# Performance work log

Hardware: AMD Instinct MI355X
Metric: run time of the kernel (lower is better)

## Reference

```python
import jax, jax.numpy as jnp
import numpy as np

B, T, V, E, H, L = 2, 1024, 32000, 768, 12, 4
HD = E // H
STD = 0.02


def setup_inputs() -> dict:
    key = jax.random.key(0)
    ks = jax.random.split(key, 16)
    inp = {}
    for i in range(L + 1):
        inp[f"t{i}"] = jax.random.randint(ks[i], (B, T), 0, V)
    inp["wte"] = jax.random.normal(ks[5], (V, E)) * STD
    inp["wpe"] = jax.random.normal(ks[6], (T, E)) * STD
    inp["ln1_w"] = jnp.ones((L, E)); inp["ln1_b"] = jnp.zeros((L, E))
    inp["ln2_w"] = jnp.ones((L, E)); inp["ln2_b"] = jnp.zeros((L, E))
    inp["attn_w"] = jax.random.normal(ks[7], (L, E, 3 * E)) * STD
    inp["attn_b"] = jnp.zeros((L, 3 * E))
    # c_proj has NANOGPT_SCALE_INIT -> std scaled by (2*L)**-0.5
    inp["proj_w"] = jax.random.normal(ks[8], (L, E, E)) * (STD * (2 * L) ** (-0.5))
    inp["proj_b"] = jnp.zeros((L, E))
    inp["fc1_w"] = jax.random.normal(ks[9], (L, E, 3 * E)) * STD
    inp["fc1_b"] = jnp.zeros((L, 3 * E))
    inp["fc2_w"] = jax.random.normal(ks[10], (L, 3 * E, E)) * STD
    inp["fc2_b"] = jnp.zeros((L, E))
    return inp


def _layernorm(x, w, b):
    mu = x.mean(-1, keepdims=True)
    var = ((x - mu) ** 2).mean(-1, keepdims=True)
    return (x - mu) / jnp.sqrt(var + 1e-5) * w + b


def _block(x, i, ln1_w, ln1_b, ln2_w, ln2_b, attn_w, attn_b, proj_w, proj_b, fc1_w, fc1_b, fc2_w, fc2_b):
    h = _layernorm(x, ln1_w[i], ln1_b[i])
    qkv = h @ attn_w[i] + attn_b[i]                       # [B,T,3E]
    q, k, v = jnp.split(qkv, 3, axis=-1)
    q = q.reshape(B, T, H, HD); k = k.reshape(B, T, H, HD); v = v.reshape(B, T, H, HD)
    # FAITHFUL quirk: original divides by d**(-0.5) == multiply by sqrt(d); no causal mask applied
    att = jnp.einsum('bqhd,bkhd->bhqk', q, k) * (HD ** 0.5)
    att = jax.nn.softmax(att, axis=-1)
    y = jnp.einsum('bhqk,bkhd->bqhd', att, v).reshape(B, T, E)
    x = x + y @ proj_w[i] + proj_b[i]
    h2 = _layernorm(x, ln2_w[i], ln2_b[i])
    return x + jax.nn.gelu(h2 @ fc1_w[i] + fc1_b[i], approximate=True) @ fc2_w[i] + fc2_b[i]


def reference(t0, t1, t2, t3, t4, wte, wpe, ln1_w, ln1_b, ln2_w, ln2_b,
              attn_w, attn_b, proj_w, proj_b, fc1_w, fc1_b, fc2_w, fc2_b):
    targets = [t0, t1, t2, t3, t4]
    pos = wpe[:T]                                         # [T,E]
    loss = jnp.float32(0.0)
    logits = None
    for i in range(L):
        x = wte[targets[i]] + pos                         # fresh embedding each layer (per original)
        x = _block(x, i, ln1_w, ln1_b, ln2_w, ln2_b, attn_w, attn_b,
                   proj_w, proj_b, fc1_w, fc1_b, fc2_w, fc2_b)
        logits = x @ wte.T                                # tied lm_head, no bias
        logp = jax.nn.log_softmax(logits, axis=-1)
        loss = loss + (-jnp.take_along_axis(logp, targets[i + 1][..., None], axis=-1).mean())
    return logits, loss
```

## Files before the change

### kernel.cpp

```cpp
#include <hip/hip_runtime.h>
#include <hip/hip_bf16.h>
#include <math.h>

#define BB 2
#define TT 1024
#define VV 32000
#define EE 768
#define HH 12
#define LL 4
#define HDIM 64
#define BT (BB*TT)
#define E3 (3*EE)

typedef __hip_bfloat16 bf16;
typedef __attribute__((ext_vector_type(8))) short bf16x8;
typedef __attribute__((ext_vector_type(4))) float f32x4;

__device__ __forceinline__ float bf2f(bf16 v) { return __bfloat162float(v); }
__device__ __forceinline__ bf16 f2bf(float v) { return __float2bfloat16(v); }

__device__ __forceinline__ void async_load16(const void* g, void* l) {
  __builtin_amdgcn_global_load_lds((const __attribute__((address_space(1))) void*)g,
                                   (__attribute__((address_space(3))) void*)l, 16, 0, 0);
}

__device__ __forceinline__ float gelu_tanh(float x) {
  float u = 0.7978845608028654f * (x + 0.044715f * x * x * x);
  return 0.5f * x * (1.0f + tanhf(u));
}


__global__ void detect_kernel(const unsigned* __restrict__ raw, int* flag, int force_bf16) {
  if (force_bf16) { *flag = 0; return; }
  *flag = (raw[0] == 0x3F800000u && raw[1] == 0x3F800000u) ? 1 : 0;
}

__global__ __launch_bounds__(256) void convert_kernel(const void* __restrict__ in,
                                                      bf16* __restrict__ out, long n,
                                                      const int* __restrict__ flag) {
  long i = (long)blockIdx.x * 256 + threadIdx.x;
  if (i >= n) return;
  int f = *flag;
  out[i] = f ? f2bf(((const float*)in)[i]) : ((const bf16*)in)[i];
}

__global__ void zero_loss_kernel(float* p) { *p = 0.f; }

__global__ void write_loss_kernel(const float* p, void* out, const int* flag) {
  if (*flag) ((float*)out)[(size_t)BT * VV] = *p;
  else       ((bf16*)out)[(size_t)BT * VV] = f2bf(*p);
}

__global__ __launch_bounds__(256) void transpose_kernel(const void* __restrict__ in,
                                                        bf16* __restrict__ out,
                                                        int R, int C, int layer,
                                                        const int* __restrict__ flag) {
  __shared__ bf16 tile[32][33];
  int f = *flag;
  const float* inf = (const float*)in + (size_t)layer * R * C;
  const bf16* inb  = (const bf16*)in  + (size_t)layer * R * C;
  int r0 = blockIdx.y * 32, c0 = blockIdx.x * 32;
#pragma unroll
  for (int i = 0; i < 4; ++i) {
    size_t idx = (size_t)(r0 + threadIdx.y + i * 8) * C + c0 + threadIdx.x;
    tile[threadIdx.y + i * 8][threadIdx.x] = f ? f2bf(inf[idx]) : inb[idx];
  }
  __syncthreads();
#pragma unroll
  for (int i = 0; i < 4; ++i) {
    int c = c0 + threadIdx.y + i * 8;
    out[(size_t)c * R + r0 + threadIdx.x] = tile[threadIdx.x][threadIdx.y + i * 8];
  }
}


__global__ __launch_bounds__(256) void embed_kernel(const int* __restrict__ tok,
                                                    const bf16* __restrict__ wte,
                                                    const bf16* __restrict__ wpe,
                                                    float* __restrict__ x) {
  int r = blockIdx.x;
  int tk = tok[r];
  int t = r & (TT - 1);
#pragma unroll
  for (int i = 0; i < 3; ++i) {
    int e = threadIdx.x + i * 256;
    x[(size_t)r * EE + e] = bf2f(wte[(size_t)tk * EE + e]) + bf2f(wpe[(size_t)t * EE + e]);
  }
}

__global__ __launch_bounds__(256) void ln_kernel(const float* __restrict__ x,
                                                 const bf16* __restrict__ wgt,
                                                 const bf16* __restrict__ bia,
                                                 bf16* __restrict__ out) {
  int r = blockIdx.x;
  const float* xr = x + (size_t)r * EE;
  int tid = threadIdx.x;
  float v0 = xr[tid], v1 = xr[tid + 256], v2 = xr[tid + 512];
  float s = v0 + v1 + v2;
  for (int o = 1; o < 64; o <<= 1) s += __shfl_xor(s, o, 64);
  __shared__ float red[4];
  int wv = tid >> 6;
  if ((tid & 63) == 0) red[wv] = s;
  __syncthreads();
  float mu = (red[0] + red[1] + red[2] + red[3]) * (1.f / 768.f);
  __syncthreads();
  float d0 = v0 - mu, d1 = v1 - mu, d2 = v2 - mu;
  float q = d0 * d0 + d1 * d1 + d2 * d2;
  for (int o = 1; o < 64; o <<= 1) q += __shfl_xor(q, o, 64);
  if ((tid & 63) == 0) red[wv] = q;
  __syncthreads();
  float var = (red[0] + red[1] + red[2] + red[3]) * (1.f / 768.f);
  float rs = rsqrtf(var + 1e-5f);
  bf16* orow = out + (size_t)r * EE;
  orow[tid]       = f2bf(d0 * rs * bf2f(wgt[tid])       + bf2f(bia[tid]));
  orow[tid + 256] = f2bf(d1 * rs * bf2f(wgt[tid + 256]) + bf2f(bia[tid + 256]));
  orow[tid + 512] = f2bf(d2 * rs * bf2f(wgt[tid + 512]) + bf2f(bia[tid + 512]));
}

__global__ __launch_bounds__(256) void split_qkv_kernel(const bf16* __restrict__ qkv,
                                                        bf16* __restrict__ Q,
                                                        bf16* __restrict__ Km,
                                                        bf16* __restrict__ Vt) {
  int idx = blockIdx.x * 256 + threadIdx.x;
  int r = idx / E3, c = idx % E3;
  int sec = c / EE, e = c % EE;
  int h = e >> 6, d = e & 63;
  int b = r >> 10, t = r & 1023;
  int bh = b * HH + h;
  bf16 v = qkv[(size_t)idx];
  if (sec == 0)      Q[((size_t)bh * TT + t) * HDIM + d] = v;
  else if (sec == 1) Km[((size_t)bh * TT + t) * HDIM + d] = v;
  else               Vt[((size_t)bh * HDIM + d) * TT + t] = v;
}


template<int BM, int BN>
__global__ __launch_bounds__(256) void gemm_bt(const bf16* __restrict__ A,
                                               const bf16* __restrict__ Bt,
                                               const bf16* __restrict__ bias,
                                               bf16* __restrict__ outb,
                                               float* __restrict__ outf,
                                               const float* __restrict__ resid,
                                               int M, int N, int K, int gelu,
                                               const int* __restrict__ oflag) {
  constexpr int IT = BM / 32;
  constexpr int JT = BN / 32;
  constexpr int ACH = BM / 64;
  constexpr int BCH = BN / 64;
  __shared__ __attribute__((aligned(16))) bf16 As[BM * 32];
  __shared__ __attribute__((aligned(16))) bf16 Bs[BN * 32];
  int f32o = (oflag != nullptr) && (*oflag != 0);
  int tid = threadIdx.x;
  int wave = tid >> 6, lane = tid & 63, low = lane & 15, quad = lane >> 4;
  int m0 = blockIdx.y * BM, n0 = blockIdx.x * BN;
  int wm = (wave >> 1) * (BM / 2), wn = (wave & 1) * (BN / 2);
  f32x4 acc[IT][JT];
  f32x4 zero = {0.f, 0.f, 0.f, 0.f};
#pragma unroll
  for (int i = 0; i < IT; ++i)
#pragma unroll
    for (int j = 0; j < JT; ++j) acc[i][j] = zero;

  for (int kb = 0; kb < K; kb += 32) {
    __syncthreads();
#pragma unroll
    for (int c = 0; c < ACH; ++c) {
      int g = c * 256 + tid;
      async_load16(A + (size_t)(m0 + (g >> 2)) * K + kb + (g & 3) * 8, (char*)As + g * 16);
    }
#pragma unroll
    for (int c = 0; c < BCH; ++c) {
      int g = c * 256 + tid;
      async_load16(Bt + (size_t)(n0 + (g >> 2)) * K + kb + (g & 3) * 8, (char*)Bs + g * 16);
    }
    __syncthreads();
    bf16x8 af[IT], bfr[JT];
#pragma unroll
    for (int i = 0; i < IT; ++i)
      af[i] = *(const bf16x8*)(As + (wm + i * 16 + low) * 32 + quad * 8);
#pragma unroll
    for (int j = 0; j < JT; ++j)
      bfr[j] = *(const bf16x8*)(Bs + (wn + j * 16 + low) * 32 + quad * 8);
#pragma unroll
    for (int i = 0; i < IT; ++i)
#pragma unroll
      for (int j = 0; j < JT; ++j)
        acc[i][j] = __builtin_amdgcn_mfma_f32_16x16x32_bf16(af[i], bfr[j], acc[i][j], 0, 0, 0);
  }

#pragma unroll
  for (int i = 0; i < IT; ++i)
#pragma unroll
    for (int j = 0; j < JT; ++j)
#pragma unroll
      for (int r = 0; r < 4; ++r) {
        int m = m0 + wm + i * 16 + quad * 4 + r;
        int n = n0 + wn + j * 16 + low;
        float v = acc[i][j][r];
        if (bias) v += bf2f(bias[n]);
        if (gelu) v = gelu_tanh(v);
        size_t idx = (size_t)m * N + n;
        if (resid) v += resid[idx];
        if (outf) outf[idx] = v;
        if (outb) {
          if (f32o) ((float*)outb)[idx] = v;
          else      outb[idx] = f2bf(v);
        }
      }
}


__global__ __launch_bounds__(64) void attn_kernel(const bf16* __restrict__ Q,
                                                  const bf16* __restrict__ Km,
                                                  const bf16* __restrict__ Vt,
                                                  bf16* __restrict__ y) {
  __shared__ __attribute__((aligned(16))) bf16 plds[16 * 32];
  int bh = blockIdx.x >> 6;
  int q0 = (blockIdx.x & 63) << 4;
  int b = bh / HH, h = bh % HH;
  int lane = threadIdx.x, low = lane & 15, quad = lane >> 4;
  const bf16* Qb = Q + (size_t)bh * TT * HDIM;
  const bf16* Kb = Km + (size_t)bh * TT * HDIM;
  const bf16* Vb = Vt + (size_t)bh * HDIM * TT;

  bf16x8 aq0 = *(const bf16x8*)(Qb + (size_t)(q0 + low) * HDIM + quad * 8);
  bf16x8 aq1 = *(const bf16x8*)(Qb + (size_t)(q0 + low) * HDIM + 32 + quad * 8);

  f32x4 o[4];
  f32x4 zero = {0.f, 0.f, 0.f, 0.f};
  float mr[4], lr[4];
#pragma unroll
  for (int r = 0; r < 4; ++r) { o[r] = zero; mr[r] = -1e30f; lr[r] = 0.f; }

  for (int kt = 0; kt < TT; kt += 32) {
    bf16x8 bk00 = *(const bf16x8*)(Kb + (size_t)(kt + low) * HDIM + quad * 8);
    bf16x8 bk01 = *(const bf16x8*)(Kb + (size_t)(kt + low) * HDIM + 32 + quad * 8);
    bf16x8 bk10 = *(const bf16x8*)(Kb + (size_t)(kt + 16 + low) * HDIM + quad * 8);
    bf16x8 bk11 = *(const bf16x8*)(Kb + (size_t)(kt + 16 + low) * HDIM + 32 + quad * 8);
    f32x4 sa = zero, sb = zero;
    sa = __builtin_amdgcn_mfma_f32_16x16x32_bf16(aq0, bk00, sa, 0, 0, 0);
    sa = __builtin_amdgcn_mfma_f32_16x16x32_bf16(aq1, bk01, sa, 0, 0, 0);
    sb = __builtin_amdgcn_mfma_f32_16x16x32_bf16(aq0, bk10, sb, 0, 0, 0);
    sb = __builtin_amdgcn_mfma_f32_16x16x32_bf16(aq1, bk11, sb, 0, 0, 0);
#pragma unroll
    for (int r = 0; r < 4; ++r) {
      float s0 = sa[r] * 8.f, s1 = sb[r] * 8.f;
      float tm = fmaxf(s0, s1);
      for (int oo = 1; oo < 16; oo <<= 1) tm = fmaxf(tm, __shfl_xor(tm, oo, 64));
      float mn = fmaxf(mr[r], tm);
      float alpha = __expf(mr[r] - mn);
      float p0 = __expf(s0 - mn), p1 = __expf(s1 - mn);
      float rs = p0 + p1;
      for (int oo = 1; oo < 16; oo <<= 1) rs += __shfl_xor(rs, oo, 64);
      lr[r] = lr[r] * alpha + rs;
      mr[r] = mn;
      o[0][r] *= alpha; o[1][r] *= alpha; o[2][r] *= alpha; o[3][r] *= alpha;
      plds[(quad * 4 + r) * 32 + low] = f2bf(p0);
      plds[(quad * 4 + r) * 32 + 16 + low] = f2bf(p1);
    }
    __syncthreads();
    bf16x8 pa = *(const bf16x8*)(plds + low * 32 + quad * 8);
#pragma unroll
    for (int fb = 0; fb < 4; ++fb) {
      bf16x8 bv = *(const bf16x8*)(Vb + (size_t)(fb * 16 + low) * TT + kt + quad * 8);
      o[fb] = __builtin_amdgcn_mfma_f32_16x16x32_bf16(pa, bv, o[fb], 0, 0, 0);
    }
    __syncthreads();
  }
#pragma unroll
  for (int fb = 0; fb < 4; ++fb)
#pragma unroll
    for (int r = 0; r < 4; ++r) {
      float val = o[fb][r] / lr[r];
      y[(size_t)(b * TT + q0 + quad * 4 + r) * EE + h * HDIM + fb * 16 + low] = f2bf(val);
    }
}


__global__ __launch_bounds__(256) void loss_kernel(const void* __restrict__ logits,
                                                   const int* __restrict__ tgt,
                                                   float* __restrict__ acc,
                                                   const int* __restrict__ flag) {
  int r = blockIdx.x;
  int f = *flag;
  const bf16* rowb = (const bf16*)logits + (size_t)r * VV;
  const float* rowf = (const float*)logits + (size_t)r * VV;
  float m = -1e30f, s = 0.f;
  for (int j = threadIdx.x; j < VV; j += 256) {
    float v = f ? rowf[j] : bf2f(rowb[j]);
    if (v > m) { s = s * __expf(m - v) + 1.f; m = v; }
    else s += __expf(v - m);
  }
  for (int o = 1; o < 64; o <<= 1) {
    float m2 = __shfl_xor(m, o, 64);
    float s2 = __shfl_xor(s, o, 64);
    float M = fmaxf(m, m2);
    s = s * __expf(m - M) + s2 * __expf(m2 - M);
    m = M;
  }
  __shared__ float sm[4], ss[4];
  int wv = threadIdx.x >> 6;
  if ((threadIdx.x & 63) == 0) { sm[wv] = m; ss[wv] = s; }
  __syncthreads();
  if (threadIdx.x == 0) {
    float M = sm[0], S = ss[0];
    for (int i = 1; i < 4; ++i) {
      float M2 = fmaxf(M, sm[i]);
      S = S * __expf(M - M2) + ss[i] * __expf(sm[i] - M2);
      M = M2;
    }
    float lse = M + logf(S);
    float tv = f ? rowf[tgt[r]] : bf2f(rowb[tgt[r]]);
    atomicAdd(acc, (lse - tv) * (1.f / (float)BT));
  }
}


extern "C" void kernel_launch(void* const* d_in, const int* in_sizes, int n_in,
                              void* d_out, int out_size, void* d_ws, size_t ws_size,
                              hipStream_t stream) {
  const int* t[5];
  for (int i = 0; i < 5; ++i) t[i] = (const int*)d_in[i];
  const void* wte_r   = d_in[5];
  const void* wpe_r   = d_in[6];
  const void* ln1w_r  = d_in[7];
  const void* ln1b_r  = d_in[8];
  const void* ln2w_r  = d_in[9];
  const void* ln2b_r  = d_in[10];
  const void* attnw_r = d_in[11];
  const void* attnb_r = d_in[12];
  const void* projw_r = d_in[13];
  const void* projb_r = d_in[14];
  const void* fc1w_r  = d_in[15];
  const void* fc1b_r  = d_in[16];
  const void* fc2w_r  = d_in[17];
  const void* fc2b_r  = d_in[18];

  char* w = (char*)d_ws;
  int* flag    = (int*)w;
  float* loss  = (float*)(w + 64); w += 256;
  float* x     = (float*)w; w += (size_t)BT * EE * 4;
  bf16* h      = (bf16*)w;  w += (size_t)BT * EE * 2;
  bf16* qkv    = (bf16*)w;  w += (size_t)BT * E3 * 2;
  bf16* g      = (bf16*)w;  w += (size_t)BT * E3 * 2;
  bf16* Q      = (bf16*)w;  w += (size_t)BT * EE * 2;
  bf16* Km     = (bf16*)w;  w += (size_t)BT * EE * 2;
  bf16* Vt     = (bf16*)w;  w += (size_t)BT * EE * 2;
  bf16* y      = (bf16*)w;  w += (size_t)BT * EE * 2;
  bf16* xb     = (bf16*)w;  w += (size_t)BT * EE * 2;
  bf16* aT     = (bf16*)w;  w += (size_t)E3 * EE * 2;
  bf16* pT     = (bf16*)w;  w += (size_t)EE * EE * 2;
  bf16* f1T    = (bf16*)w;  w += (size_t)E3 * EE * 2;
  bf16* f2T    = (bf16*)w;  w += (size_t)EE * E3 * 2;
  bf16* wpeB   = (bf16*)w;  w += (size_t)TT * EE * 2;
  bf16* ln1wB  = (bf16*)w;  w += (size_t)LL * EE * 2;
  bf16* ln1bB  = (bf16*)w;  w += (size_t)LL * EE * 2;
  bf16* ln2wB  = (bf16*)w;  w += (size_t)LL * EE * 2;
  bf16* ln2bB  = (bf16*)w;  w += (size_t)LL * EE * 2;
  bf16* attnbB = (bf16*)w;  w += (size_t)LL * E3 * 2;
  bf16* projbB = (bf16*)w;  w += (size_t)LL * EE * 2;
  bf16* fc1bB  = (bf16*)w;  w += (size_t)LL * E3 * 2;
  bf16* fc2bB  = (bf16*)w;  w += (size_t)LL * EE * 2;
  bf16* wteB   = (bf16*)w;  w += (size_t)VV * EE * 2;
  size_t need_a = (size_t)(w - (char*)d_ws);
  int modeA = ws_size >= need_a;

  bf16* out = (bf16*)d_out;
  const bf16* wte_use = modeA ? wteB : (const bf16*)wte_r;

  detect_kernel<<<1, 1, 0, stream>>>((const unsigned*)ln1w_r, flag, modeA ? 0 : 1);
  zero_loss_kernel<<<1, 1, 0, stream>>>(loss);

  if (modeA)
    convert_kernel<<<((size_t)VV * EE + 255) / 256, 256, 0, stream>>>(wte_r, wteB, (long)VV * EE, flag);
  convert_kernel<<<((size_t)TT * EE + 255) / 256, 256, 0, stream>>>(wpe_r, wpeB, (long)TT * EE, flag);
  convert_kernel<<<(LL * EE + 255) / 256, 256, 0, stream>>>(ln1w_r, ln1wB, LL * EE, flag);
  convert_kernel<<<(LL * EE + 255) / 256, 256, 0, stream>>>(ln1b_r, ln1bB, LL * EE, flag);
  convert_kernel<<<(LL * EE + 255) / 256, 256, 0, stream>>>(ln2w_r, ln2wB, LL * EE, flag);
  convert_kernel<<<(LL * EE + 255) / 256, 256, 0, stream>>>(ln2b_r, ln2bB, LL * EE, flag);
  convert_kernel<<<(LL * E3 + 255) / 256, 256, 0, stream>>>(attnb_r, attnbB, LL * E3, flag);
  convert_kernel<<<(LL * EE + 255) / 256, 256, 0, stream>>>(projb_r, projbB, LL * EE, flag);
  convert_kernel<<<(LL * E3 + 255) / 256, 256, 0, stream>>>(fc1b_r, fc1bB, LL * E3, flag);
  convert_kernel<<<(LL * EE + 255) / 256, 256, 0, stream>>>(fc2b_r, fc2bB, LL * EE, flag);

  const bf16* wpe_use = modeA ? wpeB : (const bf16*)wpe_r;

  for (int i = 0; i < LL; ++i) {
    transpose_kernel<<<dim3(E3/32, EE/32), dim3(32, 8), 0, stream>>>(attnw_r, aT, EE, E3, i, flag);
    transpose_kernel<<<dim3(EE/32, EE/32), dim3(32, 8), 0, stream>>>(projw_r, pT, EE, EE, i, flag);
    transpose_kernel<<<dim3(E3/32, EE/32), dim3(32, 8), 0, stream>>>(fc1w_r, f1T, EE, E3, i, flag);
    transpose_kernel<<<dim3(EE/32, E3/32), dim3(32, 8), 0, stream>>>(fc2w_r, f2T, E3, EE, i, flag);

    embed_kernel<<<BT, 256, 0, stream>>>(t[i], wte_use, wpe_use, x);
    ln_kernel<<<BT, 256, 0, stream>>>(x, ln1wB + i * EE, ln1bB + i * EE, h);
    gemm_bt<128, 128><<<dim3(E3/128, BT/128), 256, 0, stream>>>(
        h, aT, attnbB + i * E3, qkv, nullptr, nullptr, BT, E3, EE, 0, nullptr);
    split_qkv_kernel<<<(BT * E3) / 256, 256, 0, stream>>>(qkv, Q, Km, Vt);
    attn_kernel<<<BB * HH * (TT / 16), 64, 0, stream>>>(Q, Km, Vt, y);
    gemm_bt<64, 64><<<dim3(EE/64, BT/64), 256, 0, stream>>>(
        y, pT, projbB + i * EE, nullptr, x, x, BT, EE, EE, 0, nullptr);
    ln_kernel<<<BT, 256, 0, stream>>>(x, ln2wB + i * EE, ln2bB + i * EE, h);
    gemm_bt<128, 128><<<dim3(E3/128, BT/128), 256, 0, stream>>>(
        h, f1T, fc1bB + i * E3, g, nullptr, nullptr, BT, E3, EE, 1, nullptr);
    gemm_bt<64, 64><<<dim3(EE/64, BT/64), 256, 0, stream>>>(
        g, f2T, fc2bB + i * EE, xb, x, x, BT, EE, E3, 0, nullptr);
    gemm_bt<128, 128><<<dim3(VV/128, BT/128), 256, 0, stream>>>(
        xb, wte_use, nullptr, out, nullptr, nullptr, BT, VV, EE, 0, flag);
    loss_kernel<<<BT, 256, 0, stream>>>((const void*)out, t[i + 1], loss, flag);
  }
  write_loss_kernel<<<1, 1, 0, stream>>>(loss, (void*)d_out, flag);
}
```

Baseline: 2.503 ms.

## Fuse log-softmax partials into logits GEMM and skip unused intermediate logits writes

The lm_head GEMM epilogue now computes per-row, per-tile max and sum-exp partials and captures the target logit, so a small reduce kernel finishes the loss without re-reading the full logits. Logits are written to the output only for the final layer, because earlier layers' logits are never returned. Blocks are also remapped in column groups of 16 to improve L2 reuse of the wte tiles. The loss now uses fp32 accumulator values instead of rounded bf16 logits, and the change adds a partial buffer of BT×250 float2 values.

```diff
diff --git a/kernel.cpp b/kernel.cpp
--- a/kernel.cpp
+++ b/kernel.cpp
@@ -11,6 +11,7 @@
 #define HDIM 64
 #define BT (BB*TT)
 #define E3 (3*EE)
+#define NBLOG (VV/128)
 
 typedef __hip_bfloat16 bf16;
 typedef __attribute__((ext_vector_type(8))) short bf16x8;
@@ -134,7 +135,7 @@
 }
 
 
-template<int BM, int BN>
+template<int BM, int BN, bool LOGITS>
 __global__ __launch_bounds__(256) void gemm_bt(const bf16* __restrict__ A,
                                                const bf16* __restrict__ Bt,
                                                const bf16* __restrict__ bias,
@@ -142,7 +143,10 @@
                                                float* __restrict__ outf,
                                                const float* __restrict__ resid,
                                                int M, int N, int K, int gelu,
-                                               const int* __restrict__ oflag) {
+                                               const int* __restrict__ oflag,
+                                               const int* __restrict__ tgt,
+                                               float2* __restrict__ part,
+                                               float* __restrict__ tgtval) {
   constexpr int IT = BM / 32;
   constexpr int JT = BN / 32;
   constexpr int ACH = BM / 64;
@@ -152,7 +156,24 @@
   int f32o = (oflag != nullptr) && (*oflag != 0);
   int tid = threadIdx.x;
   int wave = tid >> 6, lane = tid & 63, low = lane & 15, quad = lane >> 4;
-  int m0 = blockIdx.y * BM, n0 = blockIdx.x * BN;
+
+  int bxn, bym;
+  if (LOGITS) {
+    int nbx = gridDim.x, nby = gridDim.y;
+    int id = blockIdx.y * nbx + blockIdx.x;
+    const int GW = 16;
+    int per = GW * nby;
+    int chunk = id / per;
+    int rem = id - chunk * per;
+    int base = chunk * GW;
+    int w = min(GW, nbx - base);
+    bxn = base + rem % w;
+    bym = rem / w;
+  } else {
+    bxn = blockIdx.x; bym = blockIdx.y;
+  }
+  int m0 = bym * BM, n0 = bxn * BN;
+
   int wm = (wave >> 1) * (BM / 2), wn = (wave & 1) * (BN / 2);
   f32x4 acc[IT][JT];
   f32x4 zero = {0.f, 0.f, 0.f, 0.f};
@@ -188,25 +209,61 @@
         acc[i][j] = __builtin_amdgcn_mfma_f32_16x16x32_bf16(af[i], bfr[j], acc[i][j], 0, 0, 0);
   }
 
-#pragma unroll
-  for (int i = 0; i < IT; ++i)
-#pragma unroll
-    for (int j = 0; j < JT; ++j)
+  if (outb || outf || bias || resid) {
+#pragma unroll
+    for (int i = 0; i < IT; ++i)
+#pragma unroll
+      for (int j = 0; j < JT; ++j)
+#pragma unroll
+        for (int r = 0; r < 4; ++r) {
+          int m = m0 + wm + i * 16 + quad * 4 + r;
+          int n = n0 + wn + j * 16 + low;
+          float v = acc[i][j][r];
+          if (bias) v += bf2f(bias[n]);
+          if (gelu) v = gelu_tanh(v);
+          size_t idx = (size_t)m * N + n;
+          if (resid) v += resid[idx];
+          if (outf) outf[idx] = v;
+          if (outb) {
+            if (f32o) ((float*)outb)[idx] = v;
+            else      outb[idx] = f2bf(v);
+          }
+        }
+  }
+
+  if constexpr (LOGITS) {
+    __shared__ float2 prt[4][BM / 2];
+#pragma unroll
+    for (int i = 0; i < IT; ++i) {
 #pragma unroll
       for (int r = 0; r < 4; ++r) {
-        int m = m0 + wm + i * 16 + quad * 4 + r;
-        int n = n0 + wn + j * 16 + low;
-        float v = acc[i][j][r];
-        if (bias) v += bf2f(bias[n]);
-        if (gelu) v = gelu_tanh(v);
-        size_t idx = (size_t)m * N + n;
-        if (resid) v += resid[idx];
-        if (outf) outf[idx] = v;
-        if (outb) {
-          if (f32o) ((float*)outb)[idx] = v;
-          else      outb[idx] = f2bf(v);
+        int mg = m0 + wm + i * 16 + quad * 4 + r;
+        int tr = tgt[mg];
+        float vmax = -1e30f;
+#pragma unroll
+        for (int j = 0; j < JT; ++j) {
+          float v = acc[i][j][r];
+          vmax = fmaxf(vmax, v);
+          int n = n0 + wn + j * 16 + low;
+          if (n == tr) tgtval[mg] = v;
         }
+        for (int oo = 1; oo < 16; oo <<= 1) vmax = fmaxf(vmax, __shfl_xor(vmax, oo, 64));
+        float se = 0.f;
+#pragma unroll
+        for (int j = 0; j < JT; ++j) se += __expf(acc[i][j][r] - vmax);
+        for (int oo = 1; oo < 16; oo <<= 1) se += __shfl_xor(se, oo, 64);
+        if (low == 0) prt[wave][i * 16 + quad * 4 + r] = make_float2(vmax, se);
       }
+    }
+    __syncthreads();
+    if (tid < BM) {
+      int half = tid >> 6, rowin = tid & 63;
+      float2 a = prt[half * 2][rowin], b = prt[half * 2 + 1][rowin];
+      float M2 = fmaxf(a.x, b.x);
+      float S = a.y * __expf(a.x - M2) + b.y * __expf(b.x - M2);
+      part[(size_t)(m0 + tid) * gridDim.x + bxn] = make_float2(M2, S);
+    }
+  }
 }
 
 
@@ -277,23 +334,20 @@
 }
 
 
-__global__ __launch_bounds__(256) void loss_kernel(const void* __restrict__ logits,
-                                                   const int* __restrict__ tgt,
-                                                   float* __restrict__ acc,
-                                                   const int* __restrict__ flag) {
+__global__ __launch_bounds__(256) void lse_reduce_kernel(const float2* __restrict__ part,
+                                                         const float* __restrict__ tgtval,
+                                                         float* __restrict__ acc, int NB) {
   int r = blockIdx.x;
-  int f = *flag;
-  const bf16* rowb = (const bf16*)logits + (size_t)r * VV;
-  const float* rowf = (const float*)logits + (size_t)r * VV;
+  const float2* p = part + (size_t)r * NB;
   float m = -1e30f, s = 0.f;
-  for (int j = threadIdx.x; j < VV; j += 256) {
-    float v = f ? rowf[j] : bf2f(rowb[j]);
-    if (v > m) { s = s * __expf(m - v) + 1.f; m = v; }
-    else s += __expf(v - m);
+  for (int j = threadIdx.x; j < NB; j += 256) {
+    float2 v = p[j];
+    float M = fmaxf(m, v.x);
+    s = s * __expf(m - M) + v.y * __expf(v.x - M);
+    m = M;
   }
   for (int o = 1; o < 64; o <<= 1) {
-    float m2 = __shfl_xor(m, o, 64);
-    float s2 = __shfl_xor(s, o, 64);
+    float m2 = __shfl_xor(m, o, 64), s2 = __shfl_xor(s, o, 64);
     float M = fmaxf(m, m2);
     s = s * __expf(m - M) + s2 * __expf(m2 - M);
     m = M;
@@ -310,8 +364,7 @@
       M = M2;
     }
     float lse = M + logf(S);
-    float tv = f ? rowf[tgt[r]] : bf2f(rowb[tgt[r]]);
-    atomicAdd(acc, (lse - tv) * (1.f / (float)BT));
+    atomicAdd(acc, (lse - tgtval[r]) * (1.f / (float)BT));
   }
 }
 
@@ -361,6 +414,8 @@
   bf16* projbB = (bf16*)w;  w += (size_t)LL * EE * 2;
   bf16* fc1bB  = (bf16*)w;  w += (size_t)LL * E3 * 2;
   bf16* fc2bB  = (bf16*)w;  w += (size_t)LL * EE * 2;
+  float2* part = (float2*)w; w += (size_t)BT * NBLOG * sizeof(float2);
+  float* tgtv  = (float*)w;  w += (size_t)BT * 4;
   bf16* wteB   = (bf16*)w;  w += (size_t)VV * EE * 2;
   size_t need_a = (size_t)(w - (char*)d_ws);
   int modeA = ws_size >= need_a;
@@ -393,20 +448,25 @@
 
     embed_kernel<<<BT, 256, 0, stream>>>(t[i], wte_use, wpe_use, x);
     ln_kernel<<<BT, 256, 0, stream>>>(x, ln1wB + i * EE, ln1bB + i * EE, h);
-    gemm_bt<128, 128><<<dim3(E3/128, BT/128), 256, 0, stream>>>(
-        h, aT, attnbB + i * E3, qkv, nullptr, nullptr, BT, E3, EE, 0, nullptr);
+    gemm_bt<128, 128, false><<<dim3(E3/128, BT/128), 256, 0, stream>>>(
+        h, aT, attnbB + i * E3, qkv, nullptr, nullptr, BT, E3, EE, 0, nullptr,
+        nullptr, nullptr, nullptr);
     split_qkv_kernel<<<(BT * E3) / 256, 256, 0, stream>>>(qkv, Q, Km, Vt);
     attn_kernel<<<BB * HH * (TT / 16), 64, 0, stream>>>(Q, Km, Vt, y);
-    gemm_bt<64, 64><<<dim3(EE/64, BT/64), 256, 0, stream>>>(
-        y, pT, projbB + i * EE, nullptr, x, x, BT, EE, EE, 0, nullptr);
+    gemm_bt<64, 64, false><<<dim3(EE/64, BT/64), 256, 0, stream>>>(
+        y, pT, projbB + i * EE, nullptr, x, x, BT, EE, EE, 0, nullptr,
+        nullptr, nullptr, nullptr);
     ln_kernel<<<BT, 256, 0, stream>>>(x, ln2wB + i * EE, ln2bB + i * EE, h);
-    gemm_bt<128, 128><<<dim3(E3/128, BT/128), 256, 0, stream>>>(
-        h, f1T, fc1bB + i * E3, g, nullptr, nullptr, BT, E3, EE, 1, nullptr);
-    gemm_bt<64, 64><<<dim3(EE/64, BT/64), 256, 0, stream>>>(
-        g, f2T, fc2bB + i * EE, xb, x, x, BT, EE, E3, 0, nullptr);
-    gemm_bt<128, 128><<<dim3(VV/128, BT/128), 256, 0, stream>>>(
-        xb, wte_use, nullptr, out, nullptr, nullptr, BT, VV, EE, 0, flag);
-    loss_kernel<<<BT, 256, 0, stream>>>((const void*)out, t[i + 1], loss, flag);
+    gemm_bt<128, 128, false><<<dim3(E3/128, BT/128), 256, 0, stream>>>(
+        h, f1T, fc1bB + i * E3, g, nullptr, nullptr, BT, E3, EE, 1, nullptr,
+        nullptr, nullptr, nullptr);
+    gemm_bt<64, 64, false><<<dim3(EE/64, BT/64), 256, 0, stream>>>(
+        g, f2T, fc2bB + i * EE, xb, x, x, BT, EE, E3, 0, nullptr,
+        nullptr, nullptr, nullptr);
+    gemm_bt<128, 128, true><<<dim3(NBLOG, BT/128), 256, 0, stream>>>(
+        xb, wte_use, nullptr, (i == LL - 1) ? out : nullptr, nullptr, nullptr,
+        BT, VV, EE, 0, flag, t[i + 1], part, tgtv);
+    lse_reduce_kernel<<<BT, 256, 0, stream>>>(part, tgtv, loss, NBLOG);
   }
   write_loss_kernel<<<1, 1, 0, stream>>>(loss, (void*)d_out, flag);
 }
```

New measurement: 2.198 ms. 12.2% less time.

## Fuse logits GEMM with partial log-softmax; skip logits writes for non-final layers

Applied to the files above, without the earlier changes.

Replaces the 128x128 logits GEMM plus full-row loss kernel with a 256x256 double-buffered, LDS-swizzled, grid-remapped GEMM. Its epilogue computes per-tile row max and sum-exp and captures the target logit. A small kernel then merges the per-tile partials into the loss. Logits are written to memory only for the last layer, since only that layer's output is returned, which removes three 32000-wide logits writes and all logits re-reads. The cost is a partials buffer, extra register pressure, and a hand-written waitcnt/barrier pipeline.

```diff
diff --git a/kernel.cpp b/kernel.cpp
--- a/kernel.cpp
+++ b/kernel.cpp
@@ -11,6 +11,7 @@
 #define HDIM 64
 #define BT (BB*TT)
 #define E3 (3*EE)
+#define NBX 125
 
 typedef __hip_bfloat16 bf16;
 typedef __attribute__((ext_vector_type(8))) short bf16x8;
@@ -141,15 +142,13 @@
                                                bf16* __restrict__ outb,
                                                float* __restrict__ outf,
                                                const float* __restrict__ resid,
-                                               int M, int N, int K, int gelu,
-                                               const int* __restrict__ oflag) {
+                                               int M, int N, int K, int gelu) {
   constexpr int IT = BM / 32;
   constexpr int JT = BN / 32;
   constexpr int ACH = BM / 64;
   constexpr int BCH = BN / 64;
   __shared__ __attribute__((aligned(16))) bf16 As[BM * 32];
   __shared__ __attribute__((aligned(16))) bf16 Bs[BN * 32];
-  int f32o = (oflag != nullptr) && (*oflag != 0);
   int tid = threadIdx.x;
   int wave = tid >> 6, lane = tid & 63, low = lane & 15, quad = lane >> 4;
   int m0 = blockIdx.y * BM, n0 = blockIdx.x * BN;
@@ -202,11 +201,156 @@
         size_t idx = (size_t)m * N + n;
         if (resid) v += resid[idx];
         if (outf) outf[idx] = v;
-        if (outb) {
-          if (f32o) ((float*)outb)[idx] = v;
-          else      outb[idx] = f2bf(v);
-        }
+        if (outb) outb[idx] = f2bf(v);
       }
+}
+
+
+__device__ __forceinline__ void stage_tile256(const bf16* __restrict__ Gp,
+                                              int kb, char* ldsTile, int tid) {
+#pragma unroll
+  for (int i = 0; i < 4; ++i) {
+    int g = i * 512 + tid;
+    int ge = g ^ (((g >> 5) & 1) << 1);
+    int row = ((ge >> 7) << 4) | ((ge >> 2) & 15);
+    int col = (((ge >> 6) & 1) << 5) | ((ge & 3) << 3);
+    async_load16(Gp + (size_t)row * EE + kb + col, ldsTile + g * 16);
+  }
+}
+
+__global__ __launch_bounds__(512, 2) void gemm256_logits(
+    const bf16* __restrict__ A,
+    const bf16* __restrict__ Bt,
+    void* __restrict__ outp,
+    const int* __restrict__ oflag,
+    const int* __restrict__ tgt,
+    float2* __restrict__ part,
+    float* __restrict__ tgtval) {
+  __shared__ __attribute__((aligned(16))) char ldsRaw[2][2][32768];
+  constexpr int NT = EE / 64;
+  int tid = threadIdx.x;
+  int wid = tid >> 6, lane = tid & 63, low = lane & 15, quad = lane >> 4;
+  int wr = wid >> 2, wc = wid & 3;
+
+  int l = blockIdx.y * NBX + blockIdx.x;
+  int l2 = (l & 7) * NBX + (l >> 3);
+  int bym = l2 / NBX, bxn = l2 - bym * NBX;
+  int m0 = bym * 256, n0 = bxn * 256;
+
+  const bf16* Ab = A + (size_t)m0 * EE;
+  const bf16* Bb = Bt + (size_t)n0 * EE;
+
+  f32x4 acc[8][4];
+  f32x4 zero = {0.f, 0.f, 0.f, 0.f};
+#pragma unroll
+  for (int mi = 0; mi < 8; ++mi)
+#pragma unroll
+    for (int nj = 0; nj < 4; ++nj) acc[mi][nj] = zero;
+
+  stage_tile256(Ab, 0, ldsRaw[0][0], tid);
+  stage_tile256(Bb, 0, ldsRaw[0][1], tid);
+
+  for (int t = 0; t < NT; ++t) {
+    int cur = t & 1;
+    if (t + 1 < NT) {
+      stage_tile256(Ab, (t + 1) * 64, ldsRaw[cur ^ 1][0], tid);
+      stage_tile256(Bb, (t + 1) * 64, ldsRaw[cur ^ 1][1], tid);
+      asm volatile("s_waitcnt vmcnt(8)" ::: "memory");
+    } else {
+      asm volatile("s_waitcnt vmcnt(0)" ::: "memory");
+    }
+    asm volatile("s_barrier" ::: "memory");
+    const char* At = ldsRaw[cur][0];
+    const char* Bs = ldsRaw[cur][1];
+#pragma unroll
+    for (int ks = 0; ks < 2; ++ks) {
+      bf16x8 af[8], bfr[4];
+#pragma unroll
+      for (int mi = 0; mi < 8; ++mi) {
+        int s = ((wr * 8 + mi) << 11) | (ks << 10) | (low << 6) | (quad << 4);
+        s ^= (low >> 3) << 5;
+        af[mi] = *(const bf16x8*)(At + s);
+      }
+#pragma unroll
+      for (int nj = 0; nj < 4; ++nj) {
+        int s = ((wc * 4 + nj) << 11) | (ks << 10) | (low << 6) | (quad << 4);
+        s ^= (low >> 3) << 5;
+        bfr[nj] = *(const bf16x8*)(Bs + s);
+      }
+      asm volatile("s_barrier" ::: "memory");
+      asm volatile("s_waitcnt lgkmcnt(0)" ::: "memory");
+      __builtin_amdgcn_sched_barrier(0);
+      __builtin_amdgcn_s_setprio(1);
+#pragma unroll
+      for (int mi = 0; mi < 8; ++mi)
+#pragma unroll
+        for (int nj = 0; nj < 4; ++nj)
+          acc[mi][nj] = __builtin_amdgcn_mfma_f32_16x16x32_bf16(af[mi], bfr[nj], acc[mi][nj], 0, 0, 0);
+      __builtin_amdgcn_s_setprio(0);
+      asm volatile("s_barrier" ::: "memory");
+    }
+  }
+
+  if (outp) {
+    int f32o = (oflag != nullptr) && (*oflag != 0);
+    if (f32o) {
+      float* of = (float*)outp;
+#pragma unroll
+      for (int mi = 0; mi < 8; ++mi)
+#pragma unroll
+        for (int nj = 0; nj < 4; ++nj)
+#pragma unroll
+          for (int r = 0; r < 4; ++r) {
+            int m = m0 + wr * 128 + mi * 16 + quad * 4 + r;
+            int n = n0 + wc * 64 + nj * 16 + low;
+            of[(size_t)m * VV + n] = acc[mi][nj][r];
+          }
+    } else {
+      bf16* ob = (bf16*)outp;
+#pragma unroll
+      for (int mi = 0; mi < 8; ++mi)
+#pragma unroll
+        for (int nj = 0; nj < 4; ++nj)
+#pragma unroll
+          for (int r = 0; r < 4; ++r) {
+            int m = m0 + wr * 128 + mi * 16 + quad * 4 + r;
+            int n = n0 + wc * 64 + nj * 16 + low;
+            ob[(size_t)m * VV + n] = f2bf(acc[mi][nj][r]);
+          }
+    }
+  }
+
+  float2* cmb = (float2*)ldsRaw;
+#pragma unroll
+  for (int mi = 0; mi < 8; ++mi) {
+#pragma unroll
+    for (int r = 0; r < 4; ++r) {
+      int rowl = wr * 128 + mi * 16 + quad * 4 + r;
+      int rowg = m0 + rowl;
+      int trg = tgt[rowg];
+      float vmax = fmaxf(fmaxf(acc[mi][0][r], acc[mi][1][r]),
+                         fmaxf(acc[mi][2][r], acc[mi][3][r]));
+#pragma unroll
+      for (int nj = 0; nj < 4; ++nj) {
+        int n = n0 + wc * 64 + nj * 16 + low;
+        if (n == trg) tgtval[rowg] = acc[mi][nj][r];
+      }
+      for (int o = 1; o < 16; o <<= 1) vmax = fmaxf(vmax, __shfl_xor(vmax, o, 64));
+      float se = 0.f;
+#pragma unroll
+      for (int nj = 0; nj < 4; ++nj) se += __expf(acc[mi][nj][r] - vmax);
+      for (int o = 1; o < 16; o <<= 1) se += __shfl_xor(se, o, 64);
+      if (low == 0) cmb[wc * 256 + rowl] = make_float2(vmax, se);
+    }
+  }
+  __syncthreads();
+  if (tid < 256) {
+    float2 a = cmb[tid], b = cmb[256 + tid], c = cmb[512 + tid], d = cmb[768 + tid];
+    float M = fmaxf(fmaxf(a.x, b.x), fmaxf(c.x, d.x));
+    float S = a.y * __expf(a.x - M) + b.y * __expf(b.x - M) +
+              c.y * __expf(c.x - M) + d.y * __expf(d.x - M);
+    part[(size_t)(m0 + tid) * NBX + bxn] = make_float2(M, S);
+  }
 }
 
 
@@ -277,23 +421,20 @@
 }
 
 
-__global__ __launch_bounds__(256) void loss_kernel(const void* __restrict__ logits,
-                                                   const int* __restrict__ tgt,
-                                                   float* __restrict__ acc,
-                                                   const int* __restrict__ flag) {
+__global__ __launch_bounds__(256) void lse_reduce_kernel(const float2* __restrict__ part,
+                                                         const float* __restrict__ tgtval,
+                                                         float* __restrict__ acc, int NB) {
   int r = blockIdx.x;
-  int f = *flag;
-  const bf16* rowb = (const bf16*)logits + (size_t)r * VV;
-  const float* rowf = (const float*)logits + (size_t)r * VV;
+  const float2* p = part + (size_t)r * NB;
   float m = -1e30f, s = 0.f;
-  for (int j = threadIdx.x; j < VV; j += 256) {
-    float v = f ? rowf[j] : bf2f(rowb[j]);
-    if (v > m) { s = s * __expf(m - v) + 1.f; m = v; }
-    else s += __expf(v - m);
+  for (int j = threadIdx.x; j < NB; j += 256) {
+    float2 v = p[j];
+    float M = fmaxf(m, v.x);
+    s = s * __expf(m - M) + v.y * __expf(v.x - M);
+    m = M;
   }
   for (int o = 1; o < 64; o <<= 1) {
-    float m2 = __shfl_xor(m, o, 64);
-    float s2 = __shfl_xor(s, o, 64);
+    float m2 = __shfl_xor(m, o, 64), s2 = __shfl_xor(s, o, 64);
     float M = fmaxf(m, m2);
     s = s * __expf(m - M) + s2 * __expf(m2 - M);
     m = M;
@@ -310,8 +451,7 @@
       M = M2;
     }
     float lse = M + logf(S);
-    float tv = f ? rowf[tgt[r]] : bf2f(rowb[tgt[r]]);
-    atomicAdd(acc, (lse - tv) * (1.f / (float)BT));
+    atomicAdd(acc, (lse - tgtval[r]) * (1.f / (float)BT));
   }
 }
 
@@ -361,6 +501,8 @@
   bf16* projbB = (bf16*)w;  w += (size_t)LL * EE * 2;
   bf16* fc1bB  = (bf16*)w;  w += (size_t)LL * E3 * 2;
   bf16* fc2bB  = (bf16*)w;  w += (size_t)LL * EE * 2;
+  float2* part = (float2*)w; w += (size_t)BT * NBX * sizeof(float2);
+  float* tgtv  = (float*)w;  w += (size_t)BT * 4;
   bf16* wteB   = (bf16*)w;  w += (size_t)VV * EE * 2;
   size_t need_a = (size_t)(w - (char*)d_ws);
   int modeA = ws_size >= need_a;
@@ -394,19 +536,19 @@
     embed_kernel<<<BT, 256, 0, stream>>>(t[i], wte_use, wpe_use, x);
     ln_kernel<<<BT, 256, 0, stream>>>(x, ln1wB + i * EE, ln1bB + i * EE, h);
     gemm_bt<128, 128><<<dim3(E3/128, BT/128), 256, 0, stream>>>(
-        h, aT, attnbB + i * E3, qkv, nullptr, nullptr, BT, E3, EE, 0, nullptr);
+        h, aT, attnbB + i * E3, qkv, nullptr, nullptr, BT, E3, EE, 0);
     split_qkv_kernel<<<(BT * E3) / 256, 256, 0, stream>>>(qkv, Q, Km, Vt);
     attn_kernel<<<BB * HH * (TT / 16), 64, 0, stream>>>(Q, Km, Vt, y);
     gemm_bt<64, 64><<<dim3(EE/64, BT/64), 256, 0, stream>>>(
-        y, pT, projbB + i * EE, nullptr, x, x, BT, EE, EE, 0, nullptr);
+        y, pT, projbB + i * EE, nullptr, x, x, BT, EE, EE, 0);
     ln_kernel<<<BT, 256, 0, stream>>>(x, ln2wB + i * EE, ln2bB + i * EE, h);
     gemm_bt<128, 128><<<dim3(E3/128, BT/128), 256, 0, stream>>>(
-        h, f1T, fc1bB + i * E3, g, nullptr, nullptr, BT, E3, EE, 1, nullptr);
+        h, f1T, fc1bB + i * E3, g, nullptr, nullptr, BT, E3, EE, 1);
     gemm_bt<64, 64><<<dim3(EE/64, BT/64), 256, 0, stream>>>(
-        g, f2T, fc2bB + i * EE, xb, x, x, BT, EE, E3, 0, nullptr);
-    gemm_bt<128, 128><<<dim3(VV/128, BT/128), 256, 0, stream>>>(
-        xb, wte_use, nullptr, out, nullptr, nullptr, BT, VV, EE, 0, flag);
-    loss_kernel<<<BT, 256, 0, stream>>>((const void*)out, t[i + 1], loss, flag);
+        g, f2T, fc2bB + i * EE, xb, x, x, BT, EE, E3, 0);
+    gemm256_logits<<<dim3(NBX, BT/256), 512, 0, stream>>>(
+        xb, wte_use, (i == LL - 1) ? (void*)out : nullptr, flag, t[i + 1], part, tgtv);
+    lse_reduce_kernel<<<BT, 256, 0, stream>>>(part, tgtv, loss, NBX);
   }
   write_loss_kernel<<<1, 1, 0, stream>>>(loss, (void*)d_out, flag);
 }
```

Result: faster. 2.065 ms (-17.5%).
